# Performance work log

Measured on AMD Instinct MI355X. Metric: run time of the kernel, lower is better.

## Reference

```python
import jax, jax.numpy as jnp
import numpy as np

B, C, D, H, W = 1, 192, 32, 32, 32
NUM_HEADS = 6
KSZ = 3
DILATIONS = (1, 2, 3)
ND = len(DILATIONS)
HPD = NUM_HEADS // ND          # heads per dilation
HEAD_DIM = C // NUM_HEADS      # 32
CPD = C // ND                  # channels per dilation = HPD * HEAD_DIM
SCALE = HEAD_DIM ** -0.5
HIDDEN = int(C * 4.0)


def setup_inputs() -> dict:
    key = jax.random.key(0)
    ks = jax.random.split(key, 12)
    s = 0.02
    return {
        "x": jax.random.normal(ks[0], (B, C, H, W, D), jnp.float32),
        "qkv_w": jax.random.normal(ks[1], (3 * C, C), jnp.float32) * s,
        "proj_w": jax.random.normal(ks[2], (C, C), jnp.float32) * s,
        "proj_b": jnp.zeros((C,), jnp.float32),
        "g1": jnp.ones((C,), jnp.float32),
        "be1": jnp.zeros((C,), jnp.float32),
        "g2": jnp.ones((C,), jnp.float32),
        "be2": jnp.zeros((C,), jnp.float32),
        "w1": jax.random.normal(ks[3], (C, HIDDEN), jnp.float32) * s,
        "b1": jnp.zeros((HIDDEN,), jnp.float32),
        "w2": jax.random.normal(ks[4], (HIDDEN, C), jnp.float32) * s,
        "b2": jnp.zeros((C,), jnp.float32),
    }


def _layernorm(x, g, b, eps=1e-5):
    mu = jnp.mean(x, -1, keepdims=True)
    var = jnp.mean(jnp.square(x - mu), -1, keepdims=True)
    return (x - mu) * jax.lax.rsqrt(var + eps) * g + b


def _unfold3d(x, k, r):
    # x: [B, c, D, H, W] -> [k^3, B, c, D, H, W] of dilated local neighborhoods
    p = r * (k - 1) // 2
    xp = jnp.pad(x, ((0, 0), (0, 0), (p, p), (p, p), (p, p)))
    d, h, w = x.shape[2:]
    sl = [xp[:, :, i:i + d, j:j + h, l:l + w]
          for i in range(0, k * r, r)
          for j in range(0, k * r, r)
          for l in range(0, k * r, r)]
    return jnp.stack(sl, 0)


def _attn(x, qkv_w, proj_w, proj_b):
    # x: [B, D, H, W, C]
    x_cf = jnp.transpose(x, (0, 4, 1, 2, 3))                   # [B,C,D,H,W]
    qkv = jnp.einsum('oc,bczyx->bozyx', qkv_w, x_cf)
    qkv = qkv.reshape(B, 3, ND, CPD, D, H, W)
    outs = []
    for i, r in enumerate(DILATIONS):
        q = qkv[:, 0, i].reshape(B, HPD, HEAD_DIM, D, H, W)
        ku = _unfold3d(qkv[:, 1, i], KSZ, r).reshape(KSZ ** 3, B, HPD, HEAD_DIM, D, H, W)
        vu = _unfold3d(qkv[:, 2, i], KSZ, r).reshape(KSZ ** 3, B, HPD, HEAD_DIM, D, H, W)
        a = jnp.einsum('bnezyx,kbnezyx->bnzyxk', q, ku) * SCALE  # [B,n,D,H,W,27]
        a = jax.nn.softmax(a, axis=-1)
        o = jnp.einsum('bnzyxk,kbnezyx->bzyxne', a, vu).reshape(B, D, H, W, CPD)
        outs.append(o)
    out = jnp.concatenate(outs, -1)                            # [B,D,H,W,C] dilation-major
    return out @ proj_w + proj_b


def reference(x, qkv_w, proj_w, proj_b, g1, be1, g2, be2, w1, b1, w2, b2):
    # x: [B, C, H, W, D] -> [B, D, H, W, C]
    h = jnp.transpose(x, (0, 4, 2, 3, 1))
    h = h + _attn(_layernorm(h, g1, be1), qkv_w, proj_w, proj_b)
    m = _layernorm(h, g2, be2)
    m = jax.nn.gelu(m @ w1 + b1, approximate=False) @ w2 + b2
    h = h + m
    return jnp.transpose(h, (0, 4, 2, 3, 1))
```

## Files before the change

### kernel.cpp

```cpp
#include <hip/hip_runtime.h>
#include <hip/hip_bf16.h>
#include <math.h>

#define NV     32768
#define HIDDEN 768
#define SCALE  0.17677669529663687f

typedef __attribute__((ext_vector_type(8))) short short8;
typedef __attribute__((ext_vector_type(4))) float floatx4;
typedef __hip_bfloat16 bf16;

__device__ __forceinline__ void gload16(const void* g, void* l) {
    __builtin_amdgcn_global_load_lds(
        (const __attribute__((address_space(1))) unsigned int*)g,
        (__attribute__((address_space(3))) unsigned int*)l, 16, 0, 0);
}

__device__ __forceinline__ float bf2f(short s) {
    unsigned u = ((unsigned)(unsigned short)s) << 16;
    return __builtin_bit_cast(float, u);
}
__device__ __forceinline__ short f2bfs(float f) {
    bf16 b = __float2bfloat16(f);
    return *reinterpret_cast<short*>(&b);
}

__global__ __launch_bounds__(256) void prep_kernel(
        const float* __restrict__ qkv_w, const float* __restrict__ proj_w,
        const float* __restrict__ w1, const float* __restrict__ w2,
        bf16* __restrict__ wqkv, bf16* __restrict__ wproj,
        bf16* __restrict__ w1t, bf16* __restrict__ w2t) {
    int i = blockIdx.x * 256 + threadIdx.x;
    if (i < 110592) {
        wqkv[i] = (bf16)qkv_w[i];
    } else if (i < 147456) {
        int j = i - 110592; int r = j / 192, c = j - r * 192;
        wproj[c * 192 + r] = (bf16)proj_w[j];
    } else if (i < 294912) {
        int j = i - 147456; int r = j / 768, c = j - r * 768;
        w1t[c * 192 + r] = (bf16)w1[j];
    } else if (i < 442368) {
        int j = i - 294912; int r = j / 192, c = j - r * 192;
        w2t[c * 768 + r] = (bf16)w2[j];
    }
}

__global__ __launch_bounds__(256) void tin_ln_kernel(
        const float* __restrict__ xin, const float* __restrict__ g,
        const float* __restrict__ be, bf16* __restrict__ h,
        bf16* __restrict__ lnb) {
    __shared__ float lds[32 * 193];
    int yx = blockIdx.x;
    int y = yx >> 5, x = yx & 31;
    for (int idx = threadIdx.x; idx < 192 * 32; idx += 256) {
        int c = idx >> 5, z = idx & 31;
        lds[z * 193 + c] = xin[(((size_t)c * 32 + y) * 32 + x) * 32 + z];
    }
    __syncthreads();
    int wave = threadIdx.x >> 6, lane = threadIdx.x & 63;
    float ga = g[lane], gb = g[lane + 64], gc = g[lane + 128];
    float ba = be[lane], bb = be[lane + 64], bc = be[lane + 128];
    for (int z = wave; z < 32; z += 4) {
        float x0 = lds[z * 193 + lane];
        float x1 = lds[z * 193 + lane + 64];
        float x2 = lds[z * 193 + lane + 128];
        float s = x0 + x1 + x2;
        #pragma unroll
        for (int m = 32; m; m >>= 1) s += __shfl_xor(s, m);
        float mu = s * (1.f / 192.f);
        float d0 = x0 - mu, d1 = x1 - mu, d2 = x2 - mu;
        float s2 = d0 * d0 + d1 * d1 + d2 * d2;
        #pragma unroll
        for (int m = 32; m; m >>= 1) s2 += __shfl_xor(s2, m);
        float rstd = rsqrtf(s2 * (1.f / 192.f) + 1e-5f);
        size_t v = (size_t)((z << 10) + (y << 5) + x) * 192;
        h[v + lane]         = (bf16)x0;
        h[v + lane + 64]    = (bf16)x1;
        h[v + lane + 128]   = (bf16)x2;
        lnb[v + lane]       = (bf16)(d0 * rstd * ga + ba);
        lnb[v + lane + 64]  = (bf16)(d1 * rstd * gb + bb);
        lnb[v + lane + 128] = (bf16)(d2 * rstd * gc + bc);
    }
}

__global__ __launch_bounds__(256) void tout_kernel(const bf16* __restrict__ h,
                                                   float* __restrict__ outp) {
    __shared__ float lds[32 * 193];
    int yx = blockIdx.x;
    int y = yx >> 5, x = yx & 31;
    for (int idx = threadIdx.x; idx < 32 * 192; idx += 256) {
        int z = idx / 192, c = idx - z * 192;
        lds[z * 193 + c] = __bfloat162float(h[((size_t)((z * 32 + y) * 32 + x)) * 192 + c]);
    }
    __syncthreads();
    for (int idx = threadIdx.x; idx < 192 * 32; idx += 256) {
        int c = idx >> 5, z = idx & 31;
        outp[(((size_t)c * 32 + y) * 32 + x) * 32 + z] = lds[z * 193 + c];
    }
}

template <int MODE>
__global__ __launch_bounds__(256, 2) void mgemm_kernel(
        const bf16* __restrict__ A,
        const bf16* __restrict__ Bw,
        void* __restrict__ Cp,
        const float* __restrict__ bias,
        const bf16* __restrict__ res,
        int M, int N, int K) {
    __shared__ short Asm[128 * 64];
    __shared__ short Bsm[64 * 64];
    const int tid = threadIdx.x;
    const int lane = tid & 63;
    const int wave = tid >> 6;
    const int wm = wave >> 1, wn = wave & 1;
    const int m0 = blockIdx.x * 128;
    const int n0 = blockIdx.y * 64;

    const int srow = lane >> 3;
    const int scol = ((lane & 7) ^ ((lane >> 3) & 7)) * 16;

    floatx4 acc[4][2] = {};

    for (int k0 = 0; k0 < K; k0 += 64) {
        #pragma unroll
        for (int s = 0; s < 4; ++s) {
            int seg = wave * 4 + s;
            const char* g = (const char*)(A + (size_t)(m0 + seg * 8 + srow) * K + k0) + scol;
            gload16(g, (char*)Asm + seg * 1024);
        }
        #pragma unroll
        for (int s = 0; s < 2; ++s) {
            int seg = wave * 2 + s;
            const char* g = (const char*)(Bw + (size_t)(n0 + seg * 8 + srow) * K + k0) + scol;
            gload16(g, (char*)Bsm + seg * 1024);
        }
        __syncthreads();
        #pragma unroll
        for (int ks = 0; ks < 2; ++ks) {
            short8 af[4], bfr[2];
            const int cb = ks * 64 + (lane >> 4) * 16;
            #pragma unroll
            for (int i = 0; i < 4; ++i) {
                int row = wm * 64 + i * 16 + (lane & 15);
                af[i] = *reinterpret_cast<const short8*>(
                    (const char*)Asm + row * 128 + (cb ^ ((row & 7) << 4)));
            }
            #pragma unroll
            for (int j = 0; j < 2; ++j) {
                int row = wn * 32 + j * 16 + (lane & 15);
                bfr[j] = *reinterpret_cast<const short8*>(
                    (const char*)Bsm + row * 128 + (cb ^ ((row & 7) << 4)));
            }
            #pragma unroll
            for (int i = 0; i < 4; ++i)
                #pragma unroll
                for (int j = 0; j < 2; ++j)
                    acc[i][j] = __builtin_amdgcn_mfma_f32_16x16x32_bf16(
                        af[i], bfr[j], acc[i][j], 0, 0, 0);
        }
        __syncthreads();
    }

    const int r4 = (lane >> 4) * 4;
    const int cc = lane & 15;
    #pragma unroll
    for (int i = 0; i < 4; ++i) {
        #pragma unroll
        for (int j = 0; j < 2; ++j) {
            int colg = n0 + wn * 32 + j * 16 + cc;
            float bv = (MODE == 1 || MODE == 2) ? bias[colg] : 0.f;
            #pragma unroll
            for (int rg = 0; rg < 4; ++rg) {
                int rowg = m0 + wm * 64 + i * 16 + r4 + rg;
                float v = acc[i][j][rg];
                if (MODE == 1 || MODE == 2) v += bv;
                if (MODE == 2) v = 0.5f * v * (1.f + erff(v * 0.70710678118654752f));
                if (MODE == 1) {
                    v += __bfloat162float(res[(size_t)rowg * N + colg]);
                    ((bf16*)Cp)[(size_t)rowg * N + colg] = (bf16)v;
                } else if (MODE == 2) {
                    ((bf16*)Cp)[(size_t)rowg * N + colg] = (bf16)v;
                } else {
                    int part = colg / 192;
                    int rem  = colg - part * 192;
                    int di   = rem >> 6, hc = rem & 63;
                    size_t addr = (size_t)part * (6 * (size_t)NV * 32)
                                + (size_t)((di << 1) + (hc >> 5)) * ((size_t)NV * 32)
                                + (size_t)rowg * 32 + (hc & 31);
                    ((bf16*)Cp)[addr] = (bf16)v;
                }
            }
        }
    }
}

__global__ __launch_bounds__(256) void projln_kernel(
        const bf16* __restrict__ A, const bf16* __restrict__ Bw,
        bf16* __restrict__ hres, bf16* __restrict__ lnout,
        const float* __restrict__ bias,
        const float* __restrict__ g2, const float* __restrict__ be2) {
    __shared__ short Asm[64 * 64];
    __shared__ short Bsm[192 * 64];
    const int tid = threadIdx.x;
    const int lane = tid & 63;
    const int wave = tid >> 6;
    const int m0 = blockIdx.x * 64;

    const int srow = lane >> 3;
    const int scol = ((lane & 7) ^ ((lane >> 3) & 7)) * 16;

    floatx4 acc[12] = {};

    for (int k0 = 0; k0 < 192; k0 += 64) {
        #pragma unroll
        for (int s = 0; s < 2; ++s) {
            int seg = wave * 2 + s;
            const char* g = (const char*)(A + (size_t)(m0 + seg * 8 + srow) * 192 + k0) + scol;
            gload16(g, (char*)Asm + seg * 1024);
        }
        #pragma unroll
        for (int s = 0; s < 6; ++s) {
            int seg = wave * 6 + s;
            const char* g = (const char*)(Bw + (size_t)(seg * 8 + srow) * 192 + k0) + scol;
            gload16(g, (char*)Bsm + seg * 1024);
        }
        __syncthreads();
        #pragma unroll
        for (int ks = 0; ks < 2; ++ks) {
            const int cb = ks * 64 + (lane >> 4) * 16;
            int arow = wave * 16 + (lane & 15);
            short8 af = *reinterpret_cast<const short8*>(
                (const char*)Asm + arow * 128 + (cb ^ ((arow & 7) << 4)));
            #pragma unroll
            for (int j = 0; j < 12; ++j) {
                int brow = j * 16 + (lane & 15);
                short8 bfr = *reinterpret_cast<const short8*>(
                    (const char*)Bsm + brow * 128 + (cb ^ ((brow & 7) << 4)));
                acc[j] = __builtin_amdgcn_mfma_f32_16x16x32_bf16(af, bfr, acc[j], 0, 0, 0);
            }
        }
        __syncthreads();
    }

    const int cc = lane & 15;
    #pragma unroll
    for (int rg = 0; rg < 4; ++rg) {
        int rowg = m0 + wave * 16 + (lane >> 4) * 4 + rg;
        float vals[12];
        float vsum = 0.f;
        #pragma unroll
        for (int j = 0; j < 12; ++j) {
            int col = j * 16 + cc;
            float v = acc[j][rg] + bias[col]
                    + __bfloat162float(hres[(size_t)rowg * 192 + col]);
            vals[j] = v;
            vsum += v;
        }
        #pragma unroll
        for (int m = 8; m; m >>= 1) vsum += __shfl_xor(vsum, m);
        float mu = vsum * (1.f / 192.f);
        float vsq = 0.f;
        #pragma unroll
        for (int j = 0; j < 12; ++j) {
            float d = vals[j] - mu;
            vsq += d * d;
        }
        #pragma unroll
        for (int m = 8; m; m >>= 1) vsq += __shfl_xor(vsq, m);
        float rstd = rsqrtf(vsq * (1.f / 192.f) + 1e-5f);
        #pragma unroll
        for (int j = 0; j < 12; ++j) {
            int col = j * 16 + cc;
            hres[(size_t)rowg * 192 + col] = (bf16)vals[j];
            lnout[(size_t)rowg * 192 + col] =
                (bf16)((vals[j] - mu) * rstd * g2[col] + be2[col]);
        }
    }
}

__global__ __launch_bounds__(256) void attn_kernel(
        const bf16* __restrict__ qa,
        const bf16* __restrict__ ka,
        const bf16* __restrict__ va,
        bf16* __restrict__ attn_out) {
    const int dh = blockIdx.y;
    const int di = dh >> 1;
    const int r  = di + 1;
    const int wave = threadIdx.x >> 6, lane = threadIdx.x & 63;
    const int yz = blockIdx.x * 4 + wave;
    const int z = yz >> 5, y = yz & 31;
    const int x = lane >> 1;
    const int v = (z << 10) + (y << 5) + x;
    const int co = (lane & 1) << 4;

    const bf16* qb = qa + (size_t)dh * NV * 32 + co;
    const bf16* kb = ka + (size_t)dh * NV * 32 + co;
    const bf16* vb = va + (size_t)dh * NV * 32 + co;

    float qf[16];
    {
        const short8* qp = reinterpret_cast<const short8*>(qb + (size_t)v * 32);
        #pragma unroll
        for (int j = 0; j < 2; ++j) {
            short8 qv = qp[j];
            #pragma unroll
            for (int u = 0; u < 8; ++u) qf[j * 8 + u] = bf2f(qv[u]);
        }
    }

    float s[27];
    #pragma unroll
    for (int kk = 0; kk < 27; ++kk) {
        const int dz = kk / 9 - 1, dy = (kk / 3) % 3 - 1, dx = kk % 3 - 1;
        int nz = z + dz * r, ny = y + dy * r, nx = x + dx * r;
        bool ok = ((unsigned)nz < 32u) & ((unsigned)ny < 32u) & ((unsigned)nx < 32u);
        int nv = ok ? v + r * ((dz << 10) + (dy << 5) + dx) : v;
        const short8* kp = reinterpret_cast<const short8*>(kb + (size_t)nv * 32);
        float d = 0.f;
        #pragma unroll
        for (int j = 0; j < 2; ++j) {
            short8 kv = kp[j];
            #pragma unroll
            for (int u = 0; u < 8; ++u) d += qf[j * 8 + u] * bf2f(kv[u]);
        }
        d += __shfl_xor(d, 1);
        s[kk] = ok ? d * SCALE : 0.f;
    }

    float mx = s[0];
    #pragma unroll
    for (int kk = 1; kk < 27; ++kk) mx = fmaxf(mx, s[kk]);

    float o[16];
    #pragma unroll
    for (int c = 0; c < 16; ++c) o[c] = 0.f;
    float denom = 0.f;
    #pragma unroll
    for (int kk = 0; kk < 27; ++kk) {
        const int dz = kk / 9 - 1, dy = (kk / 3) % 3 - 1, dx = kk % 3 - 1;
        int nz = z + dz * r, ny = y + dy * r, nx = x + dx * r;
        bool ok = ((unsigned)nz < 32u) & ((unsigned)ny < 32u) & ((unsigned)nx < 32u);
        int nv = ok ? v + r * ((dz << 10) + (dy << 5) + dx) : v;
        float p = __expf(s[kk] - mx);
        denom += p;
        float w = ok ? p : 0.f;
        const short8* vp = reinterpret_cast<const short8*>(vb + (size_t)nv * 32);
        #pragma unroll
        for (int j = 0; j < 2; ++j) {
            short8 vv = vp[j];
            #pragma unroll
            for (int u = 0; u < 8; ++u) o[j * 8 + u] += w * bf2f(vv[u]);
        }
    }
    float inv = 1.f / denom;

    bf16* op = attn_out + (size_t)v * 192 + di * 64 + (dh & 1) * 32 + co;
    #pragma unroll
    for (int j = 0; j < 2; ++j) {
        short8 st;
        #pragma unroll
        for (int u = 0; u < 8; ++u) st[u] = f2bfs(o[j * 8 + u] * inv);
        *reinterpret_cast<short8*>(op + j * 8) = st;
    }
}

extern "C" void kernel_launch(void* const* d_in, const int* in_sizes, int n_in,
                              void* d_out, int out_size, void* d_ws, size_t ws_size,
                              hipStream_t stream) {
    const float* x      = (const float*)d_in[0];
    const float* qkv_w  = (const float*)d_in[1];
    const float* proj_w = (const float*)d_in[2];
    const float* proj_b = (const float*)d_in[3];
    const float* g1     = (const float*)d_in[4];
    const float* be1    = (const float*)d_in[5];
    const float* g2     = (const float*)d_in[6];
    const float* be2    = (const float*)d_in[7];
    const float* w1     = (const float*)d_in[8];
    const float* b1     = (const float*)d_in[9];
    const float* w2     = (const float*)d_in[10];
    const float* b2     = (const float*)d_in[11];
    float* out = (float*)d_out;

    char* p = (char*)d_ws;
    bf16* h     = (bf16*)p;  p += (size_t)NV * 192 * 2;
    bf16* lnb   = (bf16*)p;  p += (size_t)NV * 192 * 2;
    bf16* qkvb  = (bf16*)p;  p += (size_t)NV * 576 * 2;
    bf16* attnb = (bf16*)p;  p += (size_t)NV * 192 * 2;
    bf16* tb    = qkvb;
    bf16* wqkv  = (bf16*)p;  p += (size_t)576 * 192 * 2;
    bf16* wproj = (bf16*)p;  p += (size_t)192 * 192 * 2;
    bf16* w1t   = (bf16*)p;  p += (size_t)768 * 192 * 2;
    bf16* w2t   = (bf16*)p;  p += (size_t)192 * 768 * 2;

    bf16* qa = qkvb;
    bf16* ka = qkvb + (size_t)6 * NV * 32;
    bf16* va = qkvb + (size_t)12 * NV * 32;

    prep_kernel<<<(442368 + 255) / 256, 256, 0, stream>>>(
        qkv_w, proj_w, w1, w2, wqkv, wproj, w1t, w2t);
    tin_ln_kernel<<<1024, 256, 0, stream>>>(x, g1, be1, h, lnb);

    mgemm_kernel<3><<<dim3(NV / 128, 576 / 64), 256, 0, stream>>>(
        lnb, wqkv, qkvb, nullptr, nullptr, NV, 576, 192);
    attn_kernel<<<dim3(256, 6), 256, 0, stream>>>(qa, ka, va, attnb);
    projln_kernel<<<NV / 64, 256, 0, stream>>>(
        attnb, wproj, h, lnb, proj_b, g2, be2);

    mgemm_kernel<2><<<dim3(NV / 128, HIDDEN / 64), 256, 0, stream>>>(
        lnb, w1t, tb, b1, nullptr, NV, HIDDEN, 192);
    mgemm_kernel<1><<<dim3(NV / 128, 192 / 64), 256, 0, stream>>>(
        tb, w2t, h, b2, h, NV, 192, HIDDEN);

    tout_kernel<<<1024, 256, 0, stream>>>(h, out);
}
```

Baseline: 161.3 us.

## Fuse attention into single pass without max subtraction and swizzle blocks

Merges the score pass and the value-accumulation pass of the local attention kernel into one loop. It drops the softmax max subtraction and uses exp2 with a prescaled constant, so K and V loads for each neighbor are issued together and the 27-entry score array goes away. Blocks are launched on a 1D grid with a swizzle that interleaves heads across groups of consecutive blocks, intended to spread L2/XCD traffic. Removing the max subtraction risks overflow if scores are large, though with small weights that is unlikely.

```diff
diff --git a/kernel.cpp b/kernel.cpp
--- a/kernel.cpp
+++ b/kernel.cpp
@@ -283,11 +283,14 @@
         const bf16* __restrict__ ka,
         const bf16* __restrict__ va,
         bf16* __restrict__ attn_out) {
-    const int dh = blockIdx.y;
+    const int lin = blockIdx.x;
+    const int swz = (lin & 7) * 192 + (lin >> 3);
+    const int dh  = swz >> 8;
+    const int yzg = swz & 255;
     const int di = dh >> 1;
     const int r  = di + 1;
     const int wave = threadIdx.x >> 6, lane = threadIdx.x & 63;
-    const int yz = blockIdx.x * 4 + wave;
+    const int yz = yzg * 4 + wave;
     const int z = yz >> 5, y = yz & 31;
     const int x = lane >> 1;
     const int v = (z << 10) + (y << 5) + x;
@@ -308,7 +311,12 @@
         }
     }
 
-    float s[27];
+    float o[16];
+    #pragma unroll
+    for (int c = 0; c < 16; ++c) o[c] = 0.f;
+    float denom = 0.f;
+    const float cexp = SCALE * 1.44269504088896f;
+
     #pragma unroll
     for (int kk = 0; kk < 27; ++kk) {
         const int dz = kk / 9 - 1, dy = (kk / 3) % 3 - 1, dx = kk % 3 - 1;
@@ -316,40 +324,23 @@
         bool ok = ((unsigned)nz < 32u) & ((unsigned)ny < 32u) & ((unsigned)nx < 32u);
         int nv = ok ? v + r * ((dz << 10) + (dy << 5) + dx) : v;
         const short8* kp = reinterpret_cast<const short8*>(kb + (size_t)nv * 32);
+        const short8* vp = reinterpret_cast<const short8*>(vb + (size_t)nv * 32);
+        short8 k0 = kp[0], k1 = kp[1];
+        short8 v0 = vp[0], v1 = vp[1];
         float d = 0.f;
         #pragma unroll
-        for (int j = 0; j < 2; ++j) {
-            short8 kv = kp[j];
-            #pragma unroll
-            for (int u = 0; u < 8; ++u) d += qf[j * 8 + u] * bf2f(kv[u]);
+        for (int u = 0; u < 8; ++u) {
+            d += qf[u]     * bf2f(k0[u]);
+            d += qf[u + 8] * bf2f(k1[u]);
         }
         d += __shfl_xor(d, 1);
-        s[kk] = ok ? d * SCALE : 0.f;
-    }
-
-    float mx = s[0];
-    #pragma unroll
-    for (int kk = 1; kk < 27; ++kk) mx = fmaxf(mx, s[kk]);
-
-    float o[16];
-    #pragma unroll
-    for (int c = 0; c < 16; ++c) o[c] = 0.f;
-    float denom = 0.f;
-    #pragma unroll
-    for (int kk = 0; kk < 27; ++kk) {
-        const int dz = kk / 9 - 1, dy = (kk / 3) % 3 - 1, dx = kk % 3 - 1;
-        int nz = z + dz * r, ny = y + dy * r, nx = x + dx * r;
-        bool ok = ((unsigned)nz < 32u) & ((unsigned)ny < 32u) & ((unsigned)nx < 32u);
-        int nv = ok ? v + r * ((dz << 10) + (dy << 5) + dx) : v;
-        float p = __expf(s[kk] - mx);
+        float p = exp2f(ok ? d * cexp : 0.f);
         denom += p;
         float w = ok ? p : 0.f;
-        const short8* vp = reinterpret_cast<const short8*>(vb + (size_t)nv * 32);
-        #pragma unroll
-        for (int j = 0; j < 2; ++j) {
-            short8 vv = vp[j];
-            #pragma unroll
-            for (int u = 0; u < 8; ++u) o[j * 8 + u] += w * bf2f(vv[u]);
+        #pragma unroll
+        for (int u = 0; u < 8; ++u) {
+            o[u]     += w * bf2f(v0[u]);
+            o[u + 8] += w * bf2f(v1[u]);
         }
     }
     float inv = 1.f / denom;
@@ -402,7 +393,7 @@
 
     mgemm_kernel<3><<<dim3(NV / 128, 576 / 64), 256, 0, stream>>>(
         lnb, wqkv, qkvb, nullptr, nullptr, NV, 576, 192);
-    attn_kernel<<<dim3(256, 6), 256, 0, stream>>>(qa, ka, va, attnb);
+    attn_kernel<<<1536, 256, 0, stream>>>(qa, ka, va, attnb);
     projln_kernel<<<NV / 64, 256, 0, stream>>>(
         attnb, wproj, h, lnb, proj_b, g2, be2);
 
```

Measured after the change: 150.0 us. 1.08x faster.
